# Kernel optimization log

Hardware: AMD Instinct MI355X
Metric: run time of the kernel (lower is better)

Reference implementation:

```python
import jax, jax.numpy as jnp
import numpy as np

K = 5          # kernel_size
ZETA = 0.15    # zeta_s
NUM_ITER = 20


def _unfold(x, k):
    # x: [B, C, H, W] -> [B, C, k*k, H, W]; zero padding, stride 1 (== nn.Unfold)
    p = k // 2
    B, C, H, W = x.shape
    xp = jnp.pad(x, ((0, 0), (0, 0), (p, p), (p, p)))
    return jnp.stack([xp[:, :, i:i + H, j:j + W]
                      for i in range(k) for j in range(k)], axis=2)


def setup_inputs() -> dict:
    key = jax.random.key(0)
    k1, k2 = jax.random.split(key)
    B, C, H, W = 4, 3, 384, 384
    img = jax.random.normal(k1, (B, C, H, W), jnp.float32)
    feat = jax.random.uniform(k2, (B, H, W), jnp.float32)
    masked_box = jnp.ones((B, H, W), jnp.float32)
    return {"img": img, "feat": feat, "masked_box": masked_box}


def reference(img, feat, masked_box):
    B, H, W = feat.shape
    img = img.astype(jnp.float32) + 10.0  # shift BEFORE zero-padded unfold (matches torch)
    unfold_img = _unfold(img, K)                          # [B, C, K2, H, W]
    # bilateral-style affinity over the K^2 window (channel-summed squared diff)
    aff = jnp.exp(-(((unfold_img - img[:, :, None]) ** 2) / (ZETA ** 2)).sum(1))  # [B, K2, H, W]
    sumz = aff.sum(1) + 1e-10                             # [B, H, W]

    x = feat * masked_box

    def step(x, _):
        ux = _unfold(x[:, None], K)[:, 0]                 # [B, K2, H, W]
        propa = (ux * aff).sum(1) / sumz                  # [B, H, W]
        return propa * masked_box, None

    x, _ = jax.lax.scan(step, x, None, length=NUM_ITER)
    return x
```

## Files before the change

kernel.cpp:

```cpp
#include <hip/hip_runtime.h>
#include <hip/hip_fp16.h>

#define BB 4
#define CC 3
#define HH 384
#define WW 384
#define HW (HH * WW)
#define NP (BB * HW)
#define KK 5
#define RR 2
#define K2 25
#define NITER 20
#define TT 48
#define KF 4
#define LR 68
#define RSTH 80
#define NTH 1024
#define IGRID 256
#define PGRID 1152
#define PCPX (PGRID / 8)
#define GUARDH 1024

static constexpr float INV_Z2 = 1.0f / (0.15f * 0.15f);


__global__ __launch_bounds__(256) void prep_sym(
    const float* __restrict__ img, const float* __restrict__ feat,
    const float* __restrict__ mask, __half* __restrict__ planes,
    float* __restrict__ invm, float* __restrict__ x0)
{
    int sbid = (blockIdx.x & 7) * PCPX + (blockIdx.x >> 3);
    int gid = sbid * 256 + threadIdx.x;
    int p0 = gid * 2;
    int b   = p0 / HW;
    int rem = p0 - b * HW;
    int h   = rem / WW;
    int wc  = rem - h * WW;

    const float* imgb = img + (size_t)b * CC * HW;
    const size_t bHW = (size_t)b * HW;

    float2 f  = *(const float2*)(feat + bHW + rem);
    float2 mk = *(const float2*)(mask + bHW + rem);
    *(float2*)(x0 + bHW + rem) = make_float2(f.x * mk.x, f.y * mk.y);

    float v0[2], v1[2], v2[2];
#pragma unroll
    for (int s = 0; s < 2; ++s) {
        v0[s] = imgb[0 * HW + rem + s] + 10.f;
        v1[s] = imgb[1 * HW + rem + s] + 10.f;
        v2[s] = imgb[2 * HW + rem + s] + 10.f;
    }

    float a[2][K2];
    float sz[2] = {1e-10f, 1e-10f};
#pragma unroll
    for (int t = 0; t < K2; ++t) {
        int dr = t / KK - RR, dc = t % KK - RR;
        int rr = h + dr;
#pragma unroll
        for (int s = 0; s < 2; ++s) {
            int cc2 = wc + s + dc;
            float av = 0.f;
            if (rr >= 0 && rr < HH && cc2 >= 0 && cc2 < WW) {
                int q = rr * WW + cc2;
                float d0 = imgb[0 * HW + q] + 10.f - v0[s];
                float d1 = imgb[1 * HW + q] + 10.f - v1[s];
                float d2 = imgb[2 * HW + q] + 10.f - v2[s];
                av = __expf(-(d0 * d0 + d1 * d1 + d2 * d2) * INV_Z2);
            }
            a[s][t] = av;
            sz[s] += av;
        }
    }
    float i0 = 1.f / sz[0], i1 = 1.f / sz[1];
    *(float2*)(invm + bHW + rem) = make_float2(mk.x * i0, mk.y * i1);
#pragma unroll
    for (int t = 13; t < K2; ++t) {
        __half2 hv = __floats2half2_rn(a[0][t], a[1][t]);
        *(__half2*)(planes + (size_t)(t - 13) * NP + bHW + rem) = hv;
    }
}

__global__ __launch_bounds__(NTH, 2) void iter4(
    const __half* __restrict__ planes, const float* __restrict__ invm,
    const float* __restrict__ xin, float* __restrict__ xout)
{
    __shared__ __half buf[2][LR][RSTH];

    const int tid = threadIdx.x;
    const int lin = (blockIdx.x & 7) * (IGRID / 8) + (blockIdx.x >> 3);
    const int b  = lin >> 6;
    const int ty = (lin >> 3) & 7;
    const int tx = lin & 7;
    const int tr0 = ty * TT, tc0 = tx * TT;
    const size_t bHW = (size_t)b * HW;

    const int row    = tid >> 4;
    const int chunk  = tid & 15;
    const int relrow = row - 8;
    const int relc0  = chunk * 4 - 8;
    const int grow = tr0 + relrow;
    const int gcol = tc0 + relc0;
    const bool inimg = ((unsigned)grow < HH) && ((unsigned)gcol <= (WW - 4));
    const int lrow = relrow + 10;
    const int hc   = relc0 + 12;

    for (int i = tid; i < LR * RSTH; i += NTH)
        ((unsigned*)buf)[i] = 0u;
    __syncthreads();

    float4 xv = make_float4(0.f, 0.f, 0.f, 0.f);
    float4 iv = make_float4(0.f, 0.f, 0.f, 0.f);
    if (inimg) {
        const size_t off = bHW + (size_t)grow * WW + gcol;
        xv = *(const float4*)(xin + off);
        iv = *(const float4*)(invm + off);
    }
    {
        union { uint2 u; __half2 h[2]; } st;
        st.h[0] = __floats2half2_rn(xv.x, xv.y);
        st.h[1] = __floats2half2_rn(xv.z, xv.w);
        *(uint2*)&buf[0][lrow][hc] = st.u;
    }

    __half2 W[K2][2];
    const __half hz = __float2half(0.f);
    if (inimg) {
        const __half* plb = planes + bHW + (size_t)grow * WW + gcol;
        W[12][0] = __floats2half2_rn(1.f, 1.f);
        W[12][1] = __floats2half2_rn(1.f, 1.f);
#pragma unroll
        for (int u = 13; u < K2; ++u) {
            const int dur = u / KK - RR;
            const int duc = u % KK - RR;
            const __half* pl = plb + (size_t)(u - 13) * NP;
            union { uint2 u2; __half2 h[2]; } ow;
            ow.u2 = *(const uint2*)pl;
            W[u][0] = ow.h[0];
            W[u][1] = ow.h[1];
            const int shift = -(dur * WW + duc);
            const bool okr = (dur == 0) || (grow >= dur);
            __half m0 = (okr && (unsigned)(gcol + 0 - duc) < WW) ? pl[shift + 0] : hz;
            __half m1 = (okr && (unsigned)(gcol + 1 - duc) < WW) ? pl[shift + 1] : hz;
            __half m2 = (okr && (unsigned)(gcol + 2 - duc) < WW) ? pl[shift + 2] : hz;
            __half m3 = (okr && (unsigned)(gcol + 3 - duc) < WW) ? pl[shift + 3] : hz;
            W[24 - u][0] = __halves2half2(m0, m1);
            W[24 - u][1] = __halves2half2(m2, m3);
        }
    } else {
#pragma unroll
        for (int t = 0; t < K2; ++t) {
            W[t][0] = __halves2half2(hz, hz);
            W[t][1] = __halves2half2(hz, hz);
        }
    }
    __syncthreads();

    int cur = 0;
    float o[4] = {0.f, 0.f, 0.f, 0.f};
#pragma unroll 1
    for (int j = 0; j < KF; ++j) {
        float acc[4] = {0.f, 0.f, 0.f, 0.f};
#pragma unroll
        for (int dr = 0; dr < KK; ++dr) {
            const __half* rp = &buf[cur][lrow - 2 + dr][hc - 4];
            union { uint2 u2; __half2 h[2]; } r0, r1, r2;
            r0.u2 = *(const uint2*)(rp);
            r1.u2 = *(const uint2*)(rp + 4);
            r2.u2 = *(const uint2*)(rp + 8);
            float xs[12];
            float2 t2;
            t2 = __half22float2(r0.h[0]); xs[0]  = t2.x; xs[1]  = t2.y;
            t2 = __half22float2(r0.h[1]); xs[2]  = t2.x; xs[3]  = t2.y;
            t2 = __half22float2(r1.h[0]); xs[4]  = t2.x; xs[5]  = t2.y;
            t2 = __half22float2(r1.h[1]); xs[6]  = t2.x; xs[7]  = t2.y;
            t2 = __half22float2(r2.h[0]); xs[8]  = t2.x; xs[9]  = t2.y;
            t2 = __half22float2(r2.h[1]); xs[10] = t2.x; xs[11] = t2.y;
#pragma unroll
            for (int dc = 0; dc < KK; ++dc) {
                const int t = dr * KK + dc;
                float2 w01 = __half22float2(W[t][0]);
                float2 w23 = __half22float2(W[t][1]);
                acc[0] = fmaf(w01.x, xs[dc + 2], acc[0]);
                acc[1] = fmaf(w01.y, xs[dc + 3], acc[1]);
                acc[2] = fmaf(w23.x, xs[dc + 4], acc[2]);
                acc[3] = fmaf(w23.y, xs[dc + 5], acc[3]);
            }
        }
        o[0] = acc[0] * iv.x; o[1] = acc[1] * iv.y;
        o[2] = acc[2] * iv.z; o[3] = acc[3] * iv.w;
        if (j < KF - 1) {
            union { uint2 u; __half2 h[2]; } st;
            st.h[0] = __floats2half2_rn(o[0], o[1]);
            st.h[1] = __floats2half2_rn(o[2], o[3]);
            *(uint2*)&buf[cur ^ 1][lrow][hc] = st.u;
            cur ^= 1;
            __syncthreads();
        }
    }

    if ((unsigned)relrow < TT && (unsigned)relc0 < TT) {
        float* dst = xout + bHW + (size_t)grow * WW + gcol;
        *(float4*)dst = make_float4(o[0], o[1], o[2], o[3]);
    }
}

extern "C" void kernel_launch(void* const* d_in, const int* in_sizes, int n_in,
                              void* d_out, int out_size, void* d_ws, size_t ws_size,
                              hipStream_t stream)
{
    const float* img  = (const float*)d_in[0];
    const float* feat = (const float*)d_in[1];
    const float* mask = (const float*)d_in[2];
    float* out = (float*)d_out;

    __half* planes = (__half*)d_ws + GUARDH;
    float* invmp = (float*)(planes + (size_t)12 * NP);
    float* xa = invmp + NP;
    float* xb = xa + NP + 64;

    prep_sym<<<PGRID, 256, 0, stream>>>(img, feat, mask, planes, invmp, xa);
    iter4<<<IGRID, NTH, 0, stream>>>(planes, invmp, xa, xb);
    iter4<<<IGRID, NTH, 0, stream>>>(planes, invmp, xb, xa);
    iter4<<<IGRID, NTH, 0, stream>>>(planes, invmp, xa, xb);
    iter4<<<IGRID, NTH, 0, stream>>>(planes, invmp, xb, xa);
    iter4<<<IGRID, NTH, 0, stream>>>(planes, invmp, xa, out);
}
```

Baseline: 157.1 us.

## Skip dead halo work, vectorize prep loads, and hoist plane loads before zero-fill

In the fused 4-step iteration kernel, each step now computes only threads whose halo region still feeds the final output, shrinking the active halo by two pixels per step. Stale values left in the unused buffer regions are never read by active threads. The plane loads are issued before the shared-memory zero fill so their latency overlaps it, and mirrored weight reads use 32-bit loads where alignment allows. The prep kernel streams image rows with float2 loads per window row instead of scalar gathers and writes the half planes inline, which removes the 2x25 affinity array held in registers.

```diff
diff --git a/kernel.cpp b/kernel.cpp
--- a/kernel.cpp
+++ b/kernel.cpp
@@ -44,42 +44,54 @@
     float2 mk = *(const float2*)(mask + bHW + rem);
     *(float2*)(x0 + bHW + rem) = make_float2(f.x * mk.x, f.y * mk.y);
 
-    float v0[2], v1[2], v2[2];
-#pragma unroll
-    for (int s = 0; s < 2; ++s) {
-        v0[s] = imgb[0 * HW + rem + s] + 10.f;
-        v1[s] = imgb[1 * HW + rem + s] + 10.f;
-        v2[s] = imgb[2 * HW + rem + s] + 10.f;
-    }
-
-    float a[2][K2];
+    float v[CC][2];
+#pragma unroll
+    for (int c = 0; c < CC; ++c) {
+        float2 cv = *(const float2*)(imgb + c * HW + rem);
+        v[c][0] = cv.x + 10.f;
+        v[c][1] = cv.y + 10.f;
+    }
+
     float sz[2] = {1e-10f, 1e-10f};
 #pragma unroll
-    for (int t = 0; t < K2; ++t) {
-        int dr = t / KK - RR, dc = t % KK - RR;
-        int rr = h + dr;
-#pragma unroll
-        for (int s = 0; s < 2; ++s) {
-            int cc2 = wc + s + dc;
-            float av = 0.f;
-            if (rr >= 0 && rr < HH && cc2 >= 0 && cc2 < WW) {
-                int q = rr * WW + cc2;
-                float d0 = imgb[0 * HW + q] + 10.f - v0[s];
-                float d1 = imgb[1 * HW + q] + 10.f - v1[s];
-                float d2 = imgb[2 * HW + q] + 10.f - v2[s];
-                av = __expf(-(d0 * d0 + d1 * d1 + d2 * d2) * INV_Z2);
-            }
-            a[s][t] = av;
-            sz[s] += av;
+    for (int dr = 0; dr < KK; ++dr) {
+        const int rr  = h + dr - RR;
+        const bool rok = (unsigned)rr < HH;
+        const int rrc = min(max(rr, 0), HH - 1);
+        float xs[CC][6];
+#pragma unroll
+        for (int c = 0; c < CC; ++c) {
+            const float* rowp = imgb + c * HW + rrc * WW;
+            float2 A = *(const float2*)(rowp + max(wc - 2, 0));
+            float2 Bv = *(const float2*)(rowp + wc);
+            float2 Cv = *(const float2*)(rowp + min(wc + 2, WW - 2));
+            xs[c][0] = A.x + 10.f;  xs[c][1] = A.y + 10.f;
+            xs[c][2] = Bv.x + 10.f; xs[c][3] = Bv.y + 10.f;
+            xs[c][4] = Cv.x + 10.f; xs[c][5] = Cv.y + 10.f;
+        }
+#pragma unroll
+        for (int dc = 0; dc < KK; ++dc) {
+            const int t = dr * KK + dc;
+            float av[2];
+#pragma unroll
+            for (int s = 0; s < 2; ++s) {
+                const int cc2 = wc + s + dc - RR;
+                const bool ok = rok && ((unsigned)cc2 < WW);
+                float d0 = xs[0][s + dc] - v[0][s];
+                float d1 = xs[1][s + dc] - v[1][s];
+                float d2 = xs[2][s + dc] - v[2][s];
+                float e = d0 * d0 + d1 * d1 + d2 * d2;
+                av[s] = ok ? __expf(-e * INV_Z2) : 0.f;
+                sz[s] += av[s];
+            }
+            if (t >= 13) {
+                __half2 hv = __floats2half2_rn(av[0], av[1]);
+                *(__half2*)(planes + (size_t)(t - 13) * NP + bHW + rem) = hv;
+            }
         }
     }
     float i0 = 1.f / sz[0], i1 = 1.f / sz[1];
     *(float2*)(invm + bHW + rem) = make_float2(mk.x * i0, mk.y * i1);
-#pragma unroll
-    for (int t = 13; t < K2; ++t) {
-        __half2 hv = __floats2half2_rn(a[0][t], a[1][t]);
-        *(__half2*)(planes + (size_t)(t - 13) * NP + bHW + rem) = hv;
-    }
 }
 
 __global__ __launch_bounds__(NTH, 2) void iter4(
@@ -106,17 +118,23 @@
     const int lrow = relrow + 10;
     const int hc   = relc0 + 12;
 
-    for (int i = tid; i < LR * RSTH; i += NTH)
-        ((unsigned*)buf)[i] = 0u;
-    __syncthreads();
-
+    uint2 own[12];
     float4 xv = make_float4(0.f, 0.f, 0.f, 0.f);
     float4 iv = make_float4(0.f, 0.f, 0.f, 0.f);
+    const __half* plb = planes + bHW + (size_t)grow * WW + gcol;
     if (inimg) {
         const size_t off = bHW + (size_t)grow * WW + gcol;
         xv = *(const float4*)(xin + off);
         iv = *(const float4*)(invm + off);
-    }
+#pragma unroll
+        for (int u = 13; u < K2; ++u)
+            own[u - 13] = *(const uint2*)(plb + (size_t)(u - 13) * NP);
+    }
+
+    for (int i = tid; i < LR * RSTH; i += NTH)
+        ((unsigned*)buf)[i] = 0u;
+    __syncthreads();
+
     {
         union { uint2 u; __half2 h[2]; } st;
         st.h[0] = __floats2half2_rn(xv.x, xv.y);
@@ -127,7 +145,6 @@
     __half2 W[K2][2];
     const __half hz = __float2half(0.f);
     if (inimg) {
-        const __half* plb = planes + bHW + (size_t)grow * WW + gcol;
         W[12][0] = __floats2half2_rn(1.f, 1.f);
         W[12][1] = __floats2half2_rn(1.f, 1.f);
 #pragma unroll
@@ -136,17 +153,27 @@
             const int duc = u % KK - RR;
             const __half* pl = plb + (size_t)(u - 13) * NP;
             union { uint2 u2; __half2 h[2]; } ow;
-            ow.u2 = *(const uint2*)pl;
+            ow.u2 = own[u - 13];
             W[u][0] = ow.h[0];
             W[u][1] = ow.h[1];
             const int shift = -(dur * WW + duc);
             const bool okr = (dur == 0) || (grow >= dur);
-            __half m0 = (okr && (unsigned)(gcol + 0 - duc) < WW) ? pl[shift + 0] : hz;
-            __half m1 = (okr && (unsigned)(gcol + 1 - duc) < WW) ? pl[shift + 1] : hz;
-            __half m2 = (okr && (unsigned)(gcol + 2 - duc) < WW) ? pl[shift + 2] : hz;
-            __half m3 = (okr && (unsigned)(gcol + 3 - duc) < WW) ? pl[shift + 3] : hz;
-            W[24 - u][0] = __halves2half2(m0, m1);
-            W[24 - u][1] = __halves2half2(m2, m3);
+            __half m[4];
+            if ((u % KK) % 2 == 0) {
+                union { unsigned u32; __half h[2]; } a0, a1;
+                a0.u32 = *(const unsigned*)(pl + shift);
+                a1.u32 = *(const unsigned*)(pl + shift + 2);
+                m[0] = a0.h[0]; m[1] = a0.h[1];
+                m[2] = a1.h[0]; m[3] = a1.h[1];
+            } else {
+                m[0] = pl[shift + 0]; m[1] = pl[shift + 1];
+                m[2] = pl[shift + 2]; m[3] = pl[shift + 3];
+            }
+#pragma unroll
+            for (int k = 0; k < 4; ++k)
+                if (!(okr && (unsigned)(gcol + k - duc) < WW)) m[k] = hz;
+            W[24 - u][0] = __halves2half2(m[0], m[1]);
+            W[24 - u][1] = __halves2half2(m[2], m[3]);
         }
     } else {
 #pragma unroll
@@ -161,40 +188,47 @@
     float o[4] = {0.f, 0.f, 0.f, 0.f};
 #pragma unroll 1
     for (int j = 0; j < KF; ++j) {
-        float acc[4] = {0.f, 0.f, 0.f, 0.f};
-#pragma unroll
-        for (int dr = 0; dr < KK; ++dr) {
-            const __half* rp = &buf[cur][lrow - 2 + dr][hc - 4];
-            union { uint2 u2; __half2 h[2]; } r0, r1, r2;
-            r0.u2 = *(const uint2*)(rp);
-            r1.u2 = *(const uint2*)(rp + 4);
-            r2.u2 = *(const uint2*)(rp + 8);
-            float xs[12];
-            float2 t2;
-            t2 = __half22float2(r0.h[0]); xs[0]  = t2.x; xs[1]  = t2.y;
-            t2 = __half22float2(r0.h[1]); xs[2]  = t2.x; xs[3]  = t2.y;
-            t2 = __half22float2(r1.h[0]); xs[4]  = t2.x; xs[5]  = t2.y;
-            t2 = __half22float2(r1.h[1]); xs[6]  = t2.x; xs[7]  = t2.y;
-            t2 = __half22float2(r2.h[0]); xs[8]  = t2.x; xs[9]  = t2.y;
-            t2 = __half22float2(r2.h[1]); xs[10] = t2.x; xs[11] = t2.y;
-#pragma unroll
-            for (int dc = 0; dc < KK; ++dc) {
-                const int t = dr * KK + dc;
-                float2 w01 = __half22float2(W[t][0]);
-                float2 w23 = __half22float2(W[t][1]);
-                acc[0] = fmaf(w01.x, xs[dc + 2], acc[0]);
-                acc[1] = fmaf(w01.y, xs[dc + 3], acc[1]);
-                acc[2] = fmaf(w23.x, xs[dc + 4], acc[2]);
-                acc[3] = fmaf(w23.y, xs[dc + 5], acc[3]);
-            }
-        }
-        o[0] = acc[0] * iv.x; o[1] = acc[1] * iv.y;
-        o[2] = acc[2] * iv.z; o[3] = acc[3] * iv.w;
+        const int rj = 2 * (KF - 1 - j);
+        const bool actj = (relrow >= -rj) && (relrow < TT + rj) &&
+                          (relc0 + 3 >= -rj) && (relc0 < TT + rj);
+        if (actj) {
+            float acc[4] = {0.f, 0.f, 0.f, 0.f};
+#pragma unroll
+            for (int dr = 0; dr < KK; ++dr) {
+                const __half* rp = &buf[cur][lrow - 2 + dr][hc - 4];
+                union { uint2 u2; __half2 h[2]; } r0, r1, r2;
+                r0.u2 = *(const uint2*)(rp);
+                r1.u2 = *(const uint2*)(rp + 4);
+                r2.u2 = *(const uint2*)(rp + 8);
+                float xs[12];
+                float2 t2;
+                t2 = __half22float2(r0.h[0]); xs[0]  = t2.x; xs[1]  = t2.y;
+                t2 = __half22float2(r0.h[1]); xs[2]  = t2.x; xs[3]  = t2.y;
+                t2 = __half22float2(r1.h[0]); xs[4]  = t2.x; xs[5]  = t2.y;
+                t2 = __half22float2(r1.h[1]); xs[6]  = t2.x; xs[7]  = t2.y;
+                t2 = __half22float2(r2.h[0]); xs[8]  = t2.x; xs[9]  = t2.y;
+                t2 = __half22float2(r2.h[1]); xs[10] = t2.x; xs[11] = t2.y;
+#pragma unroll
+                for (int dc = 0; dc < KK; ++dc) {
+                    const int t = dr * KK + dc;
+                    float2 w01 = __half22float2(W[t][0]);
+                    float2 w23 = __half22float2(W[t][1]);
+                    acc[0] = fmaf(w01.x, xs[dc + 2], acc[0]);
+                    acc[1] = fmaf(w01.y, xs[dc + 3], acc[1]);
+                    acc[2] = fmaf(w23.x, xs[dc + 4], acc[2]);
+                    acc[3] = fmaf(w23.y, xs[dc + 5], acc[3]);
+                }
+            }
+            o[0] = acc[0] * iv.x; o[1] = acc[1] * iv.y;
+            o[2] = acc[2] * iv.z; o[3] = acc[3] * iv.w;
+        }
         if (j < KF - 1) {
-            union { uint2 u; __half2 h[2]; } st;
-            st.h[0] = __floats2half2_rn(o[0], o[1]);
-            st.h[1] = __floats2half2_rn(o[2], o[3]);
-            *(uint2*)&buf[cur ^ 1][lrow][hc] = st.u;
+            if (actj) {
+                union { uint2 u; __half2 h[2]; } st;
+                st.h[0] = __floats2half2_rn(o[0], o[1]);
+                st.h[1] = __floats2half2_rn(o[2], o[3]);
+                *(uint2*)&buf[cur ^ 1][lrow][hc] = st.u;
+            }
             cur ^= 1;
             __syncthreads();
         }
```

Result: faster. 131.6 us (-16.2%).
